# Optimization experiments

Hardware: AMD Instinct MI355X
Metric: run time of the kernel (lower is better)

## Reference

```python
import jax, jax.numpy as jnp
import numpy as np

N_ITEMS = 500000
EMBED_DIM = 64
BATCH = 1024


def setup_inputs() -> dict:
    key = jax.random.key(0)
    k_emb, k_idx = jax.random.split(key)
    item_embeddings = jax.random.normal(k_emb, (N_ITEMS, EMBED_DIM), dtype=jnp.float32)
    # 1-based indices in the original API; idx-1 in [-1, N-2] wraps identically in torch/jax
    item_idx = jax.random.randint(k_idx, (BATCH,), 0, N_ITEMS, dtype=jnp.int64)
    # Approximate the module's precomputed min/max sim scores with a 256-item sample
    sample = item_embeddings[:256]  # [256, d]
    sample_sim = sample @ item_embeddings.T  # [256, N]
    min_score = jnp.min(sample_sim).reshape(1)
    max_score = jnp.max(sample_sim).reshape(1)
    return {
        "item_embeddings": item_embeddings,
        "item_idx": item_idx,
        "min_score": min_score,
        "max_score": max_score,
    }


def reference(item_embeddings, item_idx, min_score, max_score):
    # item_embeddings: [N, d]; item_idx: [B] (1-based); min/max_score: [1]
    idx = item_idx - 1  # 0-based row into the table
    item_vector = item_embeddings[idx]  # [B, d]
    sim = item_vector @ item_embeddings.T  # [B, N]
    sim = (sim - min_score[0]) / (max_score[0] - min_score[0])
    # mask self-item
    batch = idx.shape[0]
    sim = sim.at[jnp.arange(batch), idx].set(-jnp.inf)
    # top-1
    scores = jnp.max(sim, axis=1)  # [B]
    indices = jnp.argmax(sim, axis=1) + 1  # back to 1-based, [B]
    return indices, scores
```

## Files before the change

### kernel.cpp

```cpp
#include <hip/hip_runtime.h>

#define N_ITEMS 500000
#define EMBED 64
#define BATCH 1024
#define NCH ((N_ITEMS + 127) / 128)
#define CSTRIDE 256
#define CAP 4096
#define MARGIN 0.75f

typedef __attribute__((ext_vector_type(8))) __bf16 bf16x8;
typedef __attribute__((ext_vector_type(4))) float f32x4;

__device__ unsigned g_cand[BATCH * CAP];

__device__ __forceinline__ void cvt_hi(const f32x4 r0, const f32x4 r1, bf16x8& H) {
#pragma unroll
  for (int k = 0; k < 4; ++k) { H[k] = (__bf16)r0[k]; H[4 + k] = (__bf16)r1[k]; }
}

__device__ __forceinline__ float u2f(unsigned tu) {
  union { unsigned u; float f; } cv;
  cv.u = (tu & 0x80000000u) ? (tu & 0x7FFFFFFFu) : ~tu;
  return cv.f;
}

__device__ __forceinline__ unsigned f2u(float f) {
  union { float f; int i; unsigned u; } cv; cv.f = f;
  return (cv.i < 0) ? ~cv.u : (cv.u | 0x80000000u);
}

__device__ __forceinline__ float m3(float a, float b, float c) {
  return fmaxf(fmaxf(a, b), c);
}

__global__ __launch_bounds__(512, 4)
void fused_scan(const float* __restrict__ emb, const int* __restrict__ idx,
                unsigned* __restrict__ best_u, unsigned* __restrict__ cnt) {
  __shared__ unsigned short Bb[2][128 * 64];
  __shared__ int sidx[512];

  const int tid = threadIdx.x, lane = tid & 63, wv = tid >> 6;
  const int l15 = lane & 15, kq = lane >> 4;
  const int bj = blockIdx.x, rh = blockIdx.y;
  const int m0 = wv * 64, rbase = rh * 512;

  {
    int row = idx[rbase + tid] - 1;
    if (row < 0) row += N_ITEMS;
    sidx[tid] = row;
  }
  const int sr = tid >> 2, sg = tid & 3;
  __syncthreads();

  bf16x8 ah[4][2];
#pragma unroll
  for (int am = 0; am < 4; ++am) {
    const float* src = emb + (size_t)sidx[m0 + am * 16 + l15] * EMBED + kq * 8;
    cvt_hi(*(const f32x4*)(src),      *(const f32x4*)(src + 4),  ah[am][0]);
    cvt_hi(*(const f32x4*)(src + 32), *(const f32x4*)(src + 36), ah[am][1]);
  }
  const int sw = sidx[m0 + lane];

  float bs[16];
  float Tm = 3.4e38f;
#pragma unroll
  for (int sl = 0; sl < 16; ++sl) bs[sl] = -3.4e38f;

  const int nc = (NCH - 1 - bj) / CSTRIDE + 1;
  const int ntr = nc + 2;

  f32x4 raw[4];
  {
    int jr = bj * 128 + sr;
    if (jr >= N_ITEMS) jr = N_ITEMS - 1;
    const float* s = emb + (size_t)jr * EMBED + sg * 16;
#pragma unroll
    for (int i = 0; i < 4; ++i) raw[i] = *(const f32x4*)(s + 4 * i);
  }

  int p = 0;
  for (int it = 0; it < ntr; ++it) {
    const int c = (it < nc) ? bj + it * CSTRIDE : bj + (it - nc) * CSTRIDE;
    {
      bf16x8 H0, H1;
      cvt_hi(raw[0], raw[1], H0);
      cvt_hi(raw[2], raw[3], H1);
      const int g0 = (2 * sg) ^ (sr & 7), g1 = (2 * sg + 1) ^ (sr & 7);
      *(bf16x8*)(Bb[p] + sr * 64 + g0 * 8) = H0;
      *(bf16x8*)(Bb[p] + sr * 64 + g1 * 8) = H1;
    }
    __syncthreads();
    {
      const int nit = it + 1;
      if (nit < ntr) {
        const int ncn = (nit < nc) ? bj + nit * CSTRIDE : bj + (nit - nc) * CSTRIDE;
        int jr = ncn * 128 + sr;
        if (jr >= N_ITEMS) jr = N_ITEMS - 1;
        const float* s = emb + (size_t)jr * EMBED + sg * 16;
#pragma unroll
        for (int i = 0; i < 4; ++i) raw[i] = *(const f32x4*)(s + 4 * i);
      }
    }

    const bool warm = (it < 2);
    const bool masked = warm && __any((sw >> 7) == c);

#pragma unroll
    for (int bn = 0; bn < 8; ++bn) {
      const int row16 = bn * 16 + l15;
      const int fro = row16 * 64;
      bf16x8 bh0 = *(const bf16x8*)(Bb[p] + fro + ((kq ^ (row16 & 7)) << 3));
      bf16x8 bh1 = *(const bf16x8*)(Bb[p] + fro + (((4 | kq) ^ (row16 & 7)) << 3));
      const f32x4 zero = {0.f, 0.f, 0.f, 0.f};
      f32x4 acc[4];
#pragma unroll
      for (int am = 0; am < 4; ++am) {
        acc[am] = __builtin_amdgcn_mfma_f32_16x16x32_bf16(ah[am][0], bh0, zero, 0, 0, 0);
        acc[am] = __builtin_amdgcn_mfma_f32_16x16x32_bf16(ah[am][1], bh1, acc[am], 0, 0, 0);
      }

      if (warm) {
        if (!masked) {
#pragma unroll
          for (int sl = 0; sl < 16; ++sl)
            bs[sl] = fmaxf(bs[sl], acc[sl >> 2][sl & 3]);
        } else {
          const int jc = c * 128 + bn * 16 + l15;
#pragma unroll
          for (int sl = 0; sl < 16; ++sl) {
            const int self = sidx[m0 + (sl >> 2) * 16 + kq * 4 + (sl & 3)];
            float v = (jc != self) ? acc[sl >> 2][sl & 3] : -3.4e38f;
            bs[sl] = fmaxf(bs[sl], v);
          }
        }
      } else {
        float t0 = m3(acc[0][0], acc[0][1], acc[0][2]);
        float t1 = m3(acc[0][3], acc[1][0], acc[1][1]);
        float t2 = m3(acc[1][2], acc[1][3], acc[2][0]);
        float t3 = m3(acc[2][1], acc[2][2], acc[2][3]);
        float t4 = m3(acc[3][0], acc[3][1], acc[3][2]);
        float gm = fmaxf(m3(t0, t1, t2), m3(t3, t4, acc[3][3]));
        if (__any(gm >= Tm)) {
          const int jc = c * 128 + bn * 16 + l15;
#pragma unroll
          for (int sl = 0; sl < 16; ++sl) {
            if (acc[sl >> 2][sl & 3] >= bs[sl] && jc < N_ITEMS) {
              const int gr = rbase + m0 + (sl >> 2) * 16 + kq * 4 + (sl & 3);
              unsigned pos = atomicAdd(cnt + gr, 1u);
              if (pos < CAP) g_cand[gr * CAP + pos] = (unsigned)jc;
            }
          }
        }
      }
    }

    if (it == 0) {
#pragma unroll
      for (int off = 1; off < 16; off <<= 1)
#pragma unroll
        for (int sl = 0; sl < 16; ++sl)
          bs[sl] = fmaxf(bs[sl], __shfl_xor(bs[sl], off, 64));
      if (l15 == 0) {
#pragma unroll
        for (int sl = 0; sl < 16; ++sl)
          atomicMax(best_u + rbase + m0 + (sl >> 2) * 16 + kq * 4 + (sl & 3),
                    f2u(bs[sl]));
      }
    } else if (it == 1) {
#pragma unroll
      for (int off = 1; off < 16; off <<= 1)
#pragma unroll
        for (int sl = 0; sl < 16; ++sl)
          bs[sl] = fmaxf(bs[sl], __shfl_xor(bs[sl], off, 64));
#pragma unroll
      for (int sl = 0; sl < 16; ++sl) {
        unsigned g = best_u[rbase + m0 + (sl >> 2) * 16 + kq * 4 + (sl & 3)];
        float v = bs[sl];
        if (g) v = fmaxf(v, u2f(g));
        bs[sl] = v - MARGIN;
      }
      Tm = bs[0];
#pragma unroll
      for (int sl = 1; sl < 16; ++sl) Tm = fminf(Tm, bs[sl]);
    }
    p ^= 1;
  }
}

__global__ __launch_bounds__(512)
void rescore_kernel(const float* __restrict__ emb, const int* __restrict__ idx,
                    const unsigned* __restrict__ cnt,
                    const float* __restrict__ mn, const float* __restrict__ mx,
                    float* __restrict__ out) {
  const int lane = threadIdx.x & 63, wv = threadIdx.x >> 6;
  const int row = blockIdx.x * 8 + wv;
  int self = idx[row] - 1;
  if (self < 0) self += N_ITEMS;
  const float* a = emb + (size_t)self * EMBED;
  float av[EMBED];
#pragma unroll
  for (int k = 0; k < EMBED; k += 4) *(f32x4*)(av + k) = *(const f32x4*)(a + k);

  const unsigned n = cnt[row];
  float bv = -3.4e38f;
  unsigned bj = 0xFFFFFFFFu;
  if (n > CAP) {
    for (unsigned j = lane; j < N_ITEMS; j += 64) {
      if ((int)j == self) continue;
      const float* b = emb + (size_t)j * EMBED;
      float d = 0.f;
#pragma unroll
      for (int k = 0; k < EMBED; ++k) d = fmaf(av[k], b[k], d);
      if (d > bv || (d == bv && j < bj)) { bv = d; bj = j; }
    }
  } else {
    for (unsigned i = lane; i < n; i += 64) {
      unsigned j = g_cand[row * CAP + i];
      if ((int)j == self) continue;
      const float* b = emb + (size_t)j * EMBED;
      float d = 0.f;
#pragma unroll
      for (int k = 0; k < EMBED; ++k) d = fmaf(av[k], b[k], d);
      if (d > bv || (d == bv && j < bj)) { bv = d; bj = j; }
    }
  }
#pragma unroll
  for (int off = 1; off < 64; off <<= 1) {
    float ov = __shfl_xor(bv, off, 64);
    unsigned oj = (unsigned)__shfl_xor((int)bj, off, 64);
    if (ov > bv || (ov == bv && oj < bj)) { bv = ov; bj = oj; }
  }
  if (lane == 0) {
    float lo = mn[0], hi = mx[0];
    out[row] = (float)(bj + 1);
    out[BATCH + row] = (bv - lo) / (hi - lo);
  }
}

extern "C" void kernel_launch(void* const* d_in, const int* in_sizes, int n_in,
                              void* d_out, int out_size, void* d_ws, size_t ws_size,
                              hipStream_t stream) {
  const float* emb = (const float*)d_in[0];
  const int* idx   = (const int*)d_in[1];
  const float* mn  = (const float*)d_in[2];
  const float* mx  = (const float*)d_in[3];
  unsigned* ws     = (unsigned*)d_ws;
  unsigned* best_u = ws;
  unsigned* cnt    = ws + 1024;

  hipMemsetAsync(d_ws, 0, 2048 * 4, stream);

  fused_scan<<<dim3(CSTRIDE, 2), dim3(512), 0, stream>>>(emb, idx, best_u, cnt);
  rescore_kernel<<<dim3(BATCH / 8), dim3(512), 0, stream>>>(
      emb, idx, cnt, mn, mx, (float*)d_out);
}
```

Before: 298.1 us.

## Split scan into a seed kernel and a thresholded full-scan kernel

The fused scan is split into two launches of one templated kernel. MODE 0 scans the first 512 chunks and publishes per-row maxima with atomicMax. MODE 1 then scans all chunks, starting from a threshold derived from those completed global maxima minus the margin. Before, each block read best_u after only its own two warm chunks, while other blocks might not have written yet. The threshold was therefore loose and timing-dependent, which let many candidates through to the atomics and the rescore kernel. The split costs an extra kernel launch and a grid-wide barrier, and the seed chunks are still scanned twice.

```diff
diff --git a/kernel.cpp b/kernel.cpp
--- a/kernel.cpp
+++ b/kernel.cpp
@@ -4,7 +4,7 @@
 #define EMBED 64
 #define BATCH 1024
 #define NCH ((N_ITEMS + 127) / 128)
-#define CSTRIDE 256
+#define SEED_CH 512
 #define CAP 4096
 #define MARGIN 0.75f
 
@@ -24,18 +24,15 @@
   return cv.f;
 }
 
-__device__ __forceinline__ unsigned f2u(float f) {
-  union { float f; int i; unsigned u; } cv; cv.f = f;
-  return (cv.i < 0) ? ~cv.u : (cv.u | 0x80000000u);
-}
-
 __device__ __forceinline__ float m3(float a, float b, float c) {
   return fmaxf(fmaxf(a, b), c);
 }
 
+template <int MODE>
 __global__ __launch_bounds__(512, 4)
-void fused_scan(const float* __restrict__ emb, const int* __restrict__ idx,
-                unsigned* __restrict__ best_u, unsigned* __restrict__ cnt) {
+void scan_kernel(const float* __restrict__ emb, const int* __restrict__ idx,
+                 unsigned* __restrict__ best_u, unsigned* __restrict__ cnt,
+                 int climit, int stride) {
   __shared__ unsigned short Bb[2][128 * 64];
   __shared__ int sidx[512];
 
@@ -62,12 +59,23 @@
   const int sw = sidx[m0 + lane];
 
   float bs[16];
-  float Tm = 3.4e38f;
-#pragma unroll
-  for (int sl = 0; sl < 16; ++sl) bs[sl] = -3.4e38f;
-
-  const int nc = (NCH - 1 - bj) / CSTRIDE + 1;
-  const int ntr = nc + 2;
+  float Tm = 0.f;
+#pragma unroll
+  for (int am = 0; am < 4; ++am)
+#pragma unroll
+    for (int r = 0; r < 4; ++r) {
+      const int sl = am * 4 + r;
+      if (MODE == 0) {
+        bs[sl] = -3.4e38f;
+      } else {
+        bs[sl] = u2f(best_u[rbase + m0 + am * 16 + kq * 4 + r]) - MARGIN;
+      }
+    }
+  if (MODE == 1) {
+    Tm = bs[0];
+#pragma unroll
+    for (int sl = 1; sl < 16; ++sl) Tm = fminf(Tm, bs[sl]);
+  }
 
   f32x4 raw[4];
   {
@@ -79,8 +87,7 @@
   }
 
   int p = 0;
-  for (int it = 0; it < ntr; ++it) {
-    const int c = (it < nc) ? bj + it * CSTRIDE : bj + (it - nc) * CSTRIDE;
+  for (int c = bj; c < climit; c += stride) {
     {
       bf16x8 H0, H1;
       cvt_hi(raw[0], raw[1], H0);
@@ -91,10 +98,9 @@
     }
     __syncthreads();
     {
-      const int nit = it + 1;
-      if (nit < ntr) {
-        const int ncn = (nit < nc) ? bj + nit * CSTRIDE : bj + (nit - nc) * CSTRIDE;
-        int jr = ncn * 128 + sr;
+      int nc = c + stride;
+      if (nc < climit) {
+        int jr = nc * 128 + sr;
         if (jr >= N_ITEMS) jr = N_ITEMS - 1;
         const float* s = emb + (size_t)jr * EMBED + sg * 16;
 #pragma unroll
@@ -102,8 +108,7 @@
       }
     }
 
-    const bool warm = (it < 2);
-    const bool masked = warm && __any((sw >> 7) == c);
+    const bool masked = (MODE == 0) && __any((sw >> 7) == c);
 
 #pragma unroll
     for (int bn = 0; bn < 8; ++bn) {
@@ -119,7 +124,7 @@
         acc[am] = __builtin_amdgcn_mfma_f32_16x16x32_bf16(ah[am][1], bh1, acc[am], 0, 0, 0);
       }
 
-      if (warm) {
+      if (MODE == 0) {
         if (!masked) {
 #pragma unroll
           for (int sl = 0; sl < 16; ++sl)
@@ -153,37 +158,23 @@
         }
       }
     }
-
-    if (it == 0) {
-#pragma unroll
-      for (int off = 1; off < 16; off <<= 1)
-#pragma unroll
-        for (int sl = 0; sl < 16; ++sl)
-          bs[sl] = fmaxf(bs[sl], __shfl_xor(bs[sl], off, 64));
-      if (l15 == 0) {
-#pragma unroll
-        for (int sl = 0; sl < 16; ++sl)
-          atomicMax(best_u + rbase + m0 + (sl >> 2) * 16 + kq * 4 + (sl & 3),
-                    f2u(bs[sl]));
-      }
-    } else if (it == 1) {
-#pragma unroll
-      for (int off = 1; off < 16; off <<= 1)
-#pragma unroll
-        for (int sl = 0; sl < 16; ++sl)
-          bs[sl] = fmaxf(bs[sl], __shfl_xor(bs[sl], off, 64));
+    p ^= 1;
+  }
+
+  if (MODE == 0) {
+#pragma unroll
+    for (int off = 1; off < 16; off <<= 1)
+#pragma unroll
+      for (int sl = 0; sl < 16; ++sl)
+        bs[sl] = fmaxf(bs[sl], __shfl_xor(bs[sl], off, 64));
+    if (l15 == 0) {
 #pragma unroll
       for (int sl = 0; sl < 16; ++sl) {
-        unsigned g = best_u[rbase + m0 + (sl >> 2) * 16 + kq * 4 + (sl & 3)];
-        float v = bs[sl];
-        if (g) v = fmaxf(v, u2f(g));
-        bs[sl] = v - MARGIN;
-      }
-      Tm = bs[0];
-#pragma unroll
-      for (int sl = 1; sl < 16; ++sl) Tm = fminf(Tm, bs[sl]);
-    }
-    p ^= 1;
+        union { float f; int i; unsigned u; } cv; cv.f = bs[sl];
+        unsigned mu = (cv.i < 0) ? ~cv.u : (cv.u | 0x80000000u);
+        atomicMax(best_u + rbase + m0 + (sl >> 2) * 16 + kq * 4 + (sl & 3), mu);
+      }
+    }
   }
 }
 
@@ -250,7 +241,10 @@
 
   hipMemsetAsync(d_ws, 0, 2048 * 4, stream);
 
-  fused_scan<<<dim3(CSTRIDE, 2), dim3(512), 0, stream>>>(emb, idx, best_u, cnt);
+  scan_kernel<0><<<dim3(256, 2), dim3(512), 0, stream>>>(emb, idx, best_u, cnt,
+                                                         SEED_CH, 256);
+  scan_kernel<1><<<dim3(256, 2), dim3(512), 0, stream>>>(emb, idx, best_u, cnt,
+                                                         NCH, 256);
   rescore_kernel<<<dim3(BATCH / 8), dim3(512), 0, stream>>>(
       emb, idx, cnt, mn, mx, (float*)d_out);
 }
```

After: 274.4 us. 7.9% less time.
